# Performance work log

Hardware: AMD Instinct MI355X
Metric: run time of the kernel (lower is better)

Reference implementation:

```python
import jax, jax.numpy as jnp
import numpy as np

B, S, D = 4, 2048, 1024

def setup_inputs() -> dict:
    key = jax.random.key(0)
    ks = jax.random.split(key, 4)
    scale = 1.0 / np.sqrt(D)
    return {
        "x": jax.random.normal(ks[0], (B, S, D), dtype=jnp.float32),
        "Wq": jax.random.normal(ks[1], (D, D), dtype=jnp.float32) * scale,
        "bq": jnp.zeros((D,), dtype=jnp.float32),
        "Wk": jax.random.normal(ks[2], (D, D), dtype=jnp.float32) * scale,
        "bk": jnp.zeros((D,), dtype=jnp.float32),
        "Wv": jax.random.normal(ks[3], (D, D), dtype=jnp.float32) * scale,
        "bv": jnp.zeros((D,), dtype=jnp.float32),
    }

def reference(x, Wq, bq, Wk, bk, Wv, bv):
    d = x.shape[-1]
    Q = jnp.einsum('bsd,df->bsf', x, Wq) + bq  # [B,S,D]
    K = jnp.einsum('bsd,df->bsf', x, Wk) + bk
    V = jnp.einsum('bsd,df->bsf', x, Wv) + bv
    scores = jnp.einsum('bqd,bkd->bqk', Q, K) / jnp.sqrt(jnp.asarray(d, x.dtype))  # [B,S,S]
    weights = jax.nn.softmax(scores, axis=-1)
    return jnp.einsum('bqk,bkd->bqd', weights, V)  # [B,S,D]
```

## Files before the change

### kernel.cpp

```cpp
#include <hip/hip_runtime.h>
#include <stdint.h>


typedef __attribute__((ext_vector_type(8))) short bf16x8;
typedef __attribute__((ext_vector_type(4))) float f32x4;
typedef __attribute__((ext_vector_type(4))) unsigned short u16x4;
typedef __attribute__((ext_vector_type(8))) unsigned short u16x8;

__device__ __forceinline__ unsigned short f2bf(float f) {
  union { float f; unsigned u; } v; v.f = f;
  return (unsigned short)((v.u + 0x7FFFu + ((v.u >> 16) & 1u)) >> 16);
}
__device__ __forceinline__ unsigned short f2h(float f) {
  union { _Float16 h; unsigned short u; } v; v.h = (_Float16)f;
  return v.u;
}
__device__ __forceinline__ float h2f(unsigned short u) {
  union { unsigned short u; _Float16 h; } v; v.u = u;
  return (float)v.h;
}

__device__ __forceinline__ void gload16(const void* g, void* l) {
  __builtin_amdgcn_global_load_lds(
      (const __attribute__((address_space(1))) unsigned int*)g,
      (__attribute__((address_space(3))) unsigned int*)l, 16, 0, 0);
}

template <int N>
__device__ __forceinline__ void wait_vm() {
  asm volatile("s_waitcnt vmcnt(%0)" ::"n"(N) : "memory");
}

__device__ __forceinline__ int swz8(int bid, int cpx) {
  return (bid & 7) * cpx + (bid >> 3);
}

__device__ __forceinline__ f32x4 mfma16(bf16x8 a, bf16x8 b, f32x4 c) {
  return __builtin_amdgcn_mfma_f32_16x16x32_bf16(a, b, c, 0, 0, 0);
}

__device__ __forceinline__ void gemm_core(
    const unsigned short* __restrict__ A, const unsigned short* __restrict__ Bt,
    const int lda, const int ldb, const int nt,
    const long aRow0, const long bRow0, char* lds,
    f32x4 (&acc)[8][4]) {
  constexpr int A_BYTES = 256 * 64;
  constexpr int SLOT = A_BYTES + 128 * 64;
  constexpr int LA = 4, LB = 2, L = LA + LB;
  const int tid = threadIdx.x;
  const int lane = tid & 63;
  const int wid = tid >> 6;
  const int wm = wid >> 1, wn = wid & 1;
  const int l15 = lane & 15, lhi = lane >> 4;

  long goffA[LA]; int ldsoffA[LA];
#pragma unroll
  for (int j = 0; j < LA; ++j) {
    const int local = j * 4096 + tid * 16;
    const int row = local >> 6, ch = (local >> 4) & 3;
    goffA[j] = (aRow0 + row) * (long)lda + ((ch ^ ((row >> 1) & 3)) << 3);
    ldsoffA[j] = local;
  }
  long goffB[LB]; int ldsoffB[LB];
#pragma unroll
  for (int j = 0; j < LB; ++j) {
    const int local = j * 4096 + tid * 16;
    const int row = local >> 6, ch = (local >> 4) & 3;
    goffB[j] = (bRow0 + row) * (long)ldb + ((ch ^ ((row >> 1) & 3)) << 3);
    ldsoffB[j] = A_BYTES + local;
  }
  int raddrA[8];
#pragma unroll
  for (int m = 0; m < 8; ++m) {
    const int row = wm * 128 + m * 16 + l15;
    raddrA[m] = row * 64 + ((lhi ^ ((row >> 1) & 3)) << 4);
  }
  int raddrB[4];
#pragma unroll
  for (int n = 0; n < 4; ++n) {
    const int row = wn * 64 + n * 16 + l15;
    raddrB[n] = A_BYTES + row * 64 + ((lhi ^ ((row >> 1) & 3)) << 4);
  }

  const f32x4 z4 = {0.f, 0.f, 0.f, 0.f};
#pragma unroll
  for (int m = 0; m < 8; ++m)
#pragma unroll
    for (int n = 0; n < 4; ++n) acc[m][n] = z4;

  auto stage_tile = [&](int T) {
    char* dst = lds + (T % 3) * SLOT;
    const int k0 = T << 5;
#pragma unroll
    for (int j = 0; j < LA; ++j) gload16(A + goffA[j] + k0, dst + ldsoffA[j]);
#pragma unroll
    for (int j = 0; j < LB; ++j) gload16(Bt + goffB[j] + k0, dst + ldsoffB[j]);
  };

  stage_tile(0);
  stage_tile(1);
  wait_vm<L>();
  __builtin_amdgcn_s_barrier();

  for (int t = 0; t < nt; ++t) {
    const char* sb = lds + (t % 3) * SLOT;
    bf16x8 af[8], bfr[4];
#pragma unroll
    for (int n = 0; n < 4; ++n) bfr[n] = *(const bf16x8*)(sb + raddrB[n]);
#pragma unroll
    for (int m = 0; m < 8; ++m) af[m] = *(const bf16x8*)(sb + raddrA[m]);
    if (t + 2 < nt) stage_tile(t + 2);
    __builtin_amdgcn_s_setprio(1);
#pragma unroll
    for (int m = 0; m < 8; ++m)
#pragma unroll
      for (int n = 0; n < 4; ++n) acc[m][n] = mfma16(af[m], bfr[n], acc[m][n]);
    __builtin_amdgcn_s_setprio(0);
    if (t + 2 < nt) wait_vm<L>();
    else if (t + 1 < nt) wait_vm<0>();
    __builtin_amdgcn_s_barrier();
  }
}

__device__ __forceinline__ void gemm_core3(
    const unsigned short* __restrict__ A, const unsigned short* __restrict__ Bt,
    const int lda, const int ldb, const int nt64,
    const long aRow0, const long bRow0, char* lds,
    f32x4 (&acc)[8][4]) {
  constexpr int SLICE = 256 * 64;
  constexpr int A_BYTES = 2 * SLICE;
  constexpr int SLOT = 2 * A_BYTES;
  const int tid = threadIdx.x;
  const int lane = tid & 63;
  const int wid = tid >> 6;
  const int wm = wid >> 2, wn = wid & 3;
  const int l15 = lane & 15, lhi = lane >> 4;

  long goffA[2][2], goffB[2][2];
  int ldsoff[2];
#pragma unroll
  for (int j = 0; j < 2; ++j) {
    const int local = j * 8192 + tid * 16;
    const int row = local >> 6, ch = (local >> 4) & 3;
    ldsoff[j] = local;
    const int kalt = (ch ^ ((row >> 1) & 3)) << 3;
#pragma unroll
    for (int kk = 0; kk < 2; ++kk) {
      goffA[kk][j] = (aRow0 + row) * (long)lda + kk * 32 + kalt;
      goffB[kk][j] = (bRow0 + row) * (long)ldb + kk * 32 + kalt;
    }
  }
  int raddrA[8];
#pragma unroll
  for (int m = 0; m < 8; ++m) {
    const int row = wm * 128 + m * 16 + l15;
    raddrA[m] = row * 64 + ((lhi ^ ((row >> 1) & 3)) << 4);
  }
  int raddrB[4];
#pragma unroll
  for (int n = 0; n < 4; ++n) {
    const int row = wn * 64 + n * 16 + l15;
    raddrB[n] = row * 64 + ((lhi ^ ((row >> 1) & 3)) << 4);
  }

  const f32x4 z4 = {0.f, 0.f, 0.f, 0.f};
#pragma unroll
  for (int m = 0; m < 8; ++m)
#pragma unroll
    for (int n = 0; n < 4; ++n) acc[m][n] = z4;

  auto stageA = [&](int s, int kk, int T) {
    char* dst = lds + s * SLOT + kk * SLICE;
    const long k0 = (long)T << 6;
#pragma unroll
    for (int j = 0; j < 2; ++j) gload16(A + goffA[kk][j] + k0, dst + ldsoff[j]);
  };
  auto stageB = [&](int s, int kk, int T) {
    char* dst = lds + s * SLOT + A_BYTES + kk * SLICE;
    const long k0 = (long)T << 6;
#pragma unroll
    for (int j = 0; j < 2; ++j) gload16(Bt + goffB[kk][j] + k0, dst + ldsoff[j]);
  };

  stageA(0, 0, 0); stageB(0, 0, 0);
  stageA(0, 1, 0); stageB(0, 1, 0);
  wait_vm<4>();
  __builtin_amdgcn_s_barrier();

  int cur = 0;
  for (int t = 0; t < nt64; ++t) {
    const char* sb = lds + cur * SLOT;
    const int nxt = cur ^ 1;
    const bool pf = (t + 1 < nt64);
    bf16x8 a0[4], a1[4], b0[4], b1[4];
#pragma unroll
    for (int n = 0; n < 4; ++n) b0[n] = *(const bf16x8*)(sb + A_BYTES + raddrB[n]);
#pragma unroll
    for (int m = 0; m < 4; ++m) a0[m] = *(const bf16x8*)(sb + raddrA[m]);
    if (pf) stageA(nxt, 0, t + 1);
    __builtin_amdgcn_s_barrier();
    __builtin_amdgcn_s_setprio(1);
#pragma unroll
    for (int m = 0; m < 4; ++m)
#pragma unroll
      for (int n = 0; n < 4; ++n) acc[m][n] = mfma16(a0[m], b0[n], acc[m][n]);
    __builtin_amdgcn_s_setprio(0);
    __builtin_amdgcn_s_barrier();
#pragma unroll
    for (int m = 0; m < 4; ++m) a1[m] = *(const bf16x8*)(sb + raddrA[4 + m]);
    if (pf) { stageB(nxt, 0, t + 1); wait_vm<4>(); }
    else wait_vm<0>();
    __builtin_amdgcn_s_barrier();
    __builtin_amdgcn_s_setprio(1);
#pragma unroll
    for (int m = 0; m < 4; ++m)
#pragma unroll
      for (int n = 0; n < 4; ++n)
        acc[4 + m][n] = mfma16(a1[m], b0[n], acc[4 + m][n]);
    __builtin_amdgcn_s_setprio(0);
    __builtin_amdgcn_s_barrier();
#pragma unroll
    for (int n = 0; n < 4; ++n)
      b1[n] = *(const bf16x8*)(sb + A_BYTES + SLICE + raddrB[n]);
#pragma unroll
    for (int m = 0; m < 4; ++m) a0[m] = *(const bf16x8*)(sb + SLICE + raddrA[m]);
    if (pf) stageA(nxt, 1, t + 1);
    __builtin_amdgcn_s_barrier();
    __builtin_amdgcn_s_setprio(1);
#pragma unroll
    for (int m = 0; m < 4; ++m)
#pragma unroll
      for (int n = 0; n < 4; ++n) acc[m][n] = mfma16(a0[m], b1[n], acc[m][n]);
    __builtin_amdgcn_s_setprio(0);
    __builtin_amdgcn_s_barrier();
#pragma unroll
    for (int m = 0; m < 4; ++m)
      a1[m] = *(const bf16x8*)(sb + SLICE + raddrA[4 + m]);
    if (pf) { stageB(nxt, 1, t + 1); wait_vm<4>(); }
    __builtin_amdgcn_s_barrier();
    __builtin_amdgcn_s_setprio(1);
#pragma unroll
    for (int m = 0; m < 4; ++m)
#pragma unroll
      for (int n = 0; n < 4; ++n)
        acc[4 + m][n] = mfma16(a1[m], b1[n], acc[4 + m][n]);
    __builtin_amdgcn_s_setprio(0);
    __builtin_amdgcn_s_barrier();
    cur = nxt;
  }
}

__global__ __launch_bounds__(256, 2) void qkv_kernel(
    const unsigned short* __restrict__ X, const unsigned short* __restrict__ TQ,
    const unsigned short* __restrict__ TK, const unsigned short* __restrict__ TV,
    const float* __restrict__ bq, const float* __restrict__ bk,
    const float* __restrict__ bv, unsigned short* __restrict__ Q16,
    unsigned short* __restrict__ K16, unsigned short* __restrict__ VT) {
  __shared__ char lds[3 * 24576];
  const int wgid = swz8(blockIdx.x, 96);
  const int tm = wgid / 24, tn = wgid % 24;
  const int w = tn >> 3, c = tn & 7;
  const unsigned short* Bt = w == 0 ? TQ : (w == 1 ? TK : TV);
  const float* bias = w == 0 ? bq : (w == 1 ? bk : bv);

  f32x4 acc[8][4];
  gemm_core(X, Bt, 1024, 1024, 32, (long)tm * 256, (long)c * 128, lds, acc);

  const int tid = threadIdx.x, lane = tid & 63, wid = tid >> 6;
  const int wm = wid >> 1, wn = wid & 1;
  const int l15 = lane & 15, lhi = lane >> 4;
  const int rowBase = tm * 256 + wm * 128;
  const int colBase = c * 128 + wn * 64;
  if (w < 2) {
    unsigned short* C = w == 0 ? Q16 : K16;
#pragma unroll
    for (int m = 0; m < 8; ++m)
#pragma unroll
      for (int n = 0; n < 4; ++n) {
        const int col = colBase + n * 16 + l15;
        const float bvv = bias[col];
#pragma unroll
        for (int j = 0; j < 4; ++j) {
          const int row = rowBase + m * 16 + lhi * 4 + j;
          C[(long)row * 1024 + col] = f2bf(acc[m][n][j] + bvv);
        }
      }
  } else {
#pragma unroll
    for (int m = 0; m < 8; ++m)
#pragma unroll
      for (int n = 0; n < 4; ++n) {
        const int col = colBase + n * 16 + l15;
        const float bvv = bias[col];
        const int row0 = rowBase + m * 16 + lhi * 4;
        const int b = row0 >> 11, s = row0 & 2047;
        u16x4 v;
#pragma unroll
        for (int j = 0; j < 4; ++j) v[j] = f2bf(acc[m][n][j] + bvv);
        *reinterpret_cast<u16x4*>(&VT[(long)b * 2097152 + (long)col * 2048 + s]) = v;
      }
  }
}

__global__ __launch_bounds__(512, 1) void scores_kernel(
    const unsigned short* __restrict__ Q16, const unsigned short* __restrict__ K16,
    unsigned short* __restrict__ SC16) {
  extern __shared__ char lds[];
  const int wgid = swz8(blockIdx.x, 32);
  const int bz = wgid >> 6, tm = (wgid >> 3) & 7, tn = wgid & 7;
  const unsigned short* A = Q16 + (long)bz * 2097152;
  const unsigned short* Bt = K16 + (long)bz * 2097152;

  f32x4 acc[8][4];
  gemm_core3(A, Bt, 1024, 1024, 16, (long)tm * 256, (long)tn * 256, lds, acc);

  unsigned short* C = SC16 + (long)bz * 4194304;
  const int tid = threadIdx.x, lane = tid & 63, wid = tid >> 6;
  const int wm = wid >> 2, wn = wid & 3;
  const int l15 = lane & 15, lhi = lane >> 4;
  const int rowBase = tm * 256 + wm * 128;
  const int colBase = tn * 256 + wn * 64;
#pragma unroll
  for (int m = 0; m < 8; ++m)
#pragma unroll
    for (int n = 0; n < 4; ++n) {
      const int col = colBase + n * 16 + l15;
#pragma unroll
      for (int j = 0; j < 4; ++j) {
        const int row = rowBase + m * 16 + lhi * 4 + j;
        C[(long)row * 2048 + col] = f2h(acc[m][n][j] * (1.f / 32.f));
      }
    }
}

__global__ __launch_bounds__(256, 2) void pv_kernel(
    const unsigned short* __restrict__ P16, const unsigned short* __restrict__ VT,
    float* __restrict__ out) {
  __shared__ char lds[3 * 24576];
  const int wgid = swz8(blockIdx.x, 32);
  const int bz = wgid >> 6, tm = (wgid >> 3) & 7, tn = wgid & 7;
  const unsigned short* A = P16 + (long)bz * 4194304;
  const unsigned short* Bt = VT + (long)bz * 2097152;

  f32x4 acc[8][4];
  gemm_core(A, Bt, 2048, 2048, 64, (long)tm * 256, (long)tn * 128, lds, acc);

  float* C = out + (long)bz * 2097152;
  const int tid = threadIdx.x, lane = tid & 63, wid = tid >> 6;
  const int wm = wid >> 1, wn = wid & 1;
  const int l15 = lane & 15, lhi = lane >> 4;
  const int rowBase = tm * 256 + wm * 128;
  const int colBase = tn * 128 + wn * 64;
#pragma unroll
  for (int m = 0; m < 8; ++m)
#pragma unroll
    for (int n = 0; n < 4; ++n) {
      const int col = colBase + n * 16 + l15;
#pragma unroll
      for (int j = 0; j < 4; ++j) {
        const int row = rowBase + m * 16 + lhi * 4 + j;
        C[(long)row * 1024 + col] = acc[m][n][j];
      }
    }
}

__global__ __launch_bounds__(256) void cvt4(const float* __restrict__ in,
                                            unsigned short* __restrict__ out) {
  int i = blockIdx.x * 256 + threadIdx.x;
  float4 v = reinterpret_cast<const float4*>(in)[i];
  u16x4 r;
  r[0] = f2bf(v.x); r[1] = f2bf(v.y); r[2] = f2bf(v.z); r[3] = f2bf(v.w);
  reinterpret_cast<u16x4*>(out)[i] = r;
}

__global__ __launch_bounds__(256) void cvtWt(
    const float* __restrict__ w0, const float* __restrict__ w1, const float* __restrict__ w2,
    unsigned short* __restrict__ t0, unsigned short* __restrict__ t1, unsigned short* __restrict__ t2) {
  const float* w = blockIdx.y == 0 ? w0 : (blockIdx.y == 1 ? w1 : w2);
  unsigned short* t = blockIdx.y == 0 ? t0 : (blockIdx.y == 1 ? t1 : t2);
  int id = blockIdx.x * 256 + threadIdx.x;
  int k = id >> 10, n = id & 1023;
  t[n * 1024 + k] = f2bf(w[id]);
}

__global__ __launch_bounds__(256) void softmax_rows(const unsigned short* __restrict__ S,
                                                    unsigned short* __restrict__ P) {
  const long row = blockIdx.x;
  const u16x8* src = reinterpret_cast<const u16x8*>(S + row * 2048);
  const int tid = threadIdx.x;
  u16x8 a = src[tid];
  float v[8];
#pragma unroll
  for (int i = 0; i < 8; ++i) v[i] = h2f(a[i]);
  float m = v[0];
#pragma unroll
  for (int i = 1; i < 8; ++i) m = fmaxf(m, v[i]);
#pragma unroll
  for (int o = 32; o > 0; o >>= 1) m = fmaxf(m, __shfl_xor(m, o));
  __shared__ float red[8];
  const int wid = tid >> 6, lane = tid & 63;
  if (lane == 0) red[wid] = m;
  __syncthreads();
  m = fmaxf(fmaxf(red[0], red[1]), fmaxf(red[2], red[3]));
  float s = 0.f;
#pragma unroll
  for (int i = 0; i < 8; ++i) { v[i] = __expf(v[i] - m); s += v[i]; }
#pragma unroll
  for (int o = 32; o > 0; o >>= 1) s += __shfl_xor(s, o);
  if (lane == 0) red[4 + wid] = s;
  __syncthreads();
  s = (red[4] + red[5]) + (red[6] + red[7]);
  const float inv = 1.f / s;
  u16x8 p;
#pragma unroll
  for (int i = 0; i < 8; ++i) p[i] = f2bf(v[i] * inv);
  reinterpret_cast<u16x8*>(P + row * 2048)[tid] = p;
}

extern "C" void kernel_launch(void* const* d_in, const int* in_sizes, int n_in,
                              void* d_out, int out_size, void* d_ws, size_t ws_size,
                              hipStream_t stream) {
  const float* x  = (const float*)d_in[0];
  const float* Wq = (const float*)d_in[1];
  const float* bq = (const float*)d_in[2];
  const float* Wk = (const float*)d_in[3];
  const float* bk = (const float*)d_in[4];
  const float* Wv = (const float*)d_in[5];
  const float* bv = (const float*)d_in[6];
  float* out = (float*)d_out;

  char* ws = (char*)d_ws;
  const size_t MB = 1024 * 1024;
  unsigned short* X16 = (unsigned short*)(ws);
  unsigned short* TQ  = (unsigned short*)(ws + 16 * MB);
  unsigned short* TK  = (unsigned short*)(ws + 18 * MB);
  unsigned short* TV  = (unsigned short*)(ws + 20 * MB);
  unsigned short* Q16 = (unsigned short*)(ws + 22 * MB);
  unsigned short* K16 = (unsigned short*)(ws + 38 * MB);
  unsigned short* VT  = (unsigned short*)(ws + 54 * MB);
  unsigned short* SC16 = (unsigned short*)(ws + 70 * MB);
  unsigned short* P16 = Q16;

  static bool attr_set = false;
  if (!attr_set) {
    hipFuncSetAttribute(reinterpret_cast<const void*>(scores_kernel),
                        hipFuncAttributeMaxDynamicSharedMemorySize, 131072);
    attr_set = true;
  }

  cvt4<<<8192, 256, 0, stream>>>(x, X16);
  cvtWt<<<dim3(4096, 3), 256, 0, stream>>>(Wq, Wk, Wv, TQ, TK, TV);

  qkv_kernel<<<768, 256, 0, stream>>>(X16, TQ, TK, TV, bq, bk, bv, Q16, K16, VT);
  scores_kernel<<<256, 512, 131072, stream>>>(Q16, K16, SC16);
  softmax_rows<<<4 * 2048, 256, 0, stream>>>(SC16, P16);
  pv_kernel<<<256, 256, 0, stream>>>(P16, VT, out);

  (void)in_sizes; (void)n_in; (void)out_size; (void)ws_size;
}
```

Before: 174.4 us.

## Split PV tile across 8 waves and fuse conversion kernels into one launch

The PV GEMM moves from 256 threads holding 8x4 accumulator fragments per wave to 512 threads holding 4x4. The block tile stays 256x128, so each wave carries half the accumulators and the CU gets more waves to hide latency. A dedicated staging core splits the global-to-LDS loads for the new thread count. Separately, the x conversion and the weight-transpose conversion are merged into one kernel launch, with each weight block handling four elements per thread, to cut launch overhead. The cost is more LDS read traffic per MFMA in the PV loop, and the weight transpose still uses uncoalesced stores.

```diff
diff --git a/kernel.cpp b/kernel.cpp
--- a/kernel.cpp
+++ b/kernel.cpp
@@ -122,6 +122,87 @@
   }
 }
 
+__device__ __forceinline__ void gemm_core_pv(
+    const unsigned short* __restrict__ A, const unsigned short* __restrict__ Bt,
+    const int lda, const int ldb, const int nt,
+    const long aRow0, const long bRow0, char* lds,
+    f32x4 (&acc)[4][4]) {
+  constexpr int A_BYTES = 256 * 64;
+  constexpr int SLOT = A_BYTES + 128 * 64;
+  constexpr int LA = 2, LB = 1, L = LA + LB;
+  const int tid = threadIdx.x;
+  const int lane = tid & 63;
+  const int wid = tid >> 6;
+  const int wm = wid >> 1, wn = wid & 1;
+  const int l15 = lane & 15, lhi = lane >> 4;
+
+  long goffA[LA]; int ldsoffA[LA];
+#pragma unroll
+  for (int j = 0; j < LA; ++j) {
+    const int local = j * 8192 + tid * 16;
+    const int row = local >> 6, ch = (local >> 4) & 3;
+    goffA[j] = (aRow0 + row) * (long)lda + ((ch ^ ((row >> 1) & 3)) << 3);
+    ldsoffA[j] = local;
+  }
+  long goffB; int ldsoffB;
+  {
+    const int local = tid * 16;
+    const int row = local >> 6, ch = (local >> 4) & 3;
+    goffB = (bRow0 + row) * (long)ldb + ((ch ^ ((row >> 1) & 3)) << 3);
+    ldsoffB = A_BYTES + local;
+  }
+  int raddrA[4];
+#pragma unroll
+  for (int m = 0; m < 4; ++m) {
+    const int row = wm * 64 + m * 16 + l15;
+    raddrA[m] = row * 64 + ((lhi ^ ((row >> 1) & 3)) << 4);
+  }
+  int raddrB[4];
+#pragma unroll
+  for (int n = 0; n < 4; ++n) {
+    const int row = wn * 64 + n * 16 + l15;
+    raddrB[n] = A_BYTES + row * 64 + ((lhi ^ ((row >> 1) & 3)) << 4);
+  }
+
+  const f32x4 z4 = {0.f, 0.f, 0.f, 0.f};
+#pragma unroll
+  for (int m = 0; m < 4; ++m)
+#pragma unroll
+    for (int n = 0; n < 4; ++n) acc[m][n] = z4;
+
+  auto stage_tile = [&](int T) {
+    char* dst = lds + (T % 3) * SLOT;
+    const int k0 = T << 5;
+#pragma unroll
+    for (int j = 0; j < LA; ++j) gload16(A + goffA[j] + k0, dst + ldsoffA[j]);
+    gload16(Bt + goffB + k0, dst + ldsoffB);
+  };
+
+  stage_tile(0);
+  stage_tile(1);
+  wait_vm<L>();
+  __builtin_amdgcn_s_barrier();
+
+  for (int t = 0; t < nt; ++t) {
+    const char* sb = lds + (t % 3) * SLOT;
+    bf16x8 af[4], bfr[4];
+#pragma unroll
+    for (int n = 0; n < 4; ++n) bfr[n] = *(const bf16x8*)(sb + raddrB[n]);
+#pragma unroll
+    for (int m = 0; m < 4; ++m) af[m] = *(const bf16x8*)(sb + raddrA[m]);
+    if (t + 2 < nt) stage_tile(t + 2);
+    __builtin_amdgcn_s_setprio(1);
+#pragma unroll
+    for (int m = 0; m < 4; ++m)
+#pragma unroll
+      for (int n = 0; n < 4; ++n) acc[m][n] = mfma16(af[m], bfr[n], acc[m][n]);
+    __builtin_amdgcn_s_setprio(0);
+    if (t + 2 < nt) wait_vm<L>();
+    else if (t + 1 < nt) wait_vm<0>();
+    __builtin_amdgcn_s_barrier();
+  }
+}
+
 __device__ __forceinline__ void gemm_core3(
     const unsigned short* __restrict__ A, const unsigned short* __restrict__ Bt,
     const int lda, const int ldb, const int nt64,
@@ -333,7 +414,7 @@
     }
 }
 
-__global__ __launch_bounds__(256, 2) void pv_kernel(
+__global__ __launch_bounds__(512, 1) void pv_kernel(
     const unsigned short* __restrict__ P16, const unsigned short* __restrict__ VT,
     float* __restrict__ out) {
   __shared__ char lds[3 * 24576];
@@ -342,17 +423,17 @@
   const unsigned short* A = P16 + (long)bz * 4194304;
   const unsigned short* Bt = VT + (long)bz * 2097152;
 
-  f32x4 acc[8][4];
-  gemm_core(A, Bt, 2048, 2048, 64, (long)tm * 256, (long)tn * 128, lds, acc);
+  f32x4 acc[4][4];
+  gemm_core_pv(A, Bt, 2048, 2048, 64, (long)tm * 256, (long)tn * 128, lds, acc);
 
   float* C = out + (long)bz * 2097152;
   const int tid = threadIdx.x, lane = tid & 63, wid = tid >> 6;
   const int wm = wid >> 1, wn = wid & 1;
   const int l15 = lane & 15, lhi = lane >> 4;
-  const int rowBase = tm * 256 + wm * 128;
+  const int rowBase = tm * 256 + wm * 64;
   const int colBase = tn * 128 + wn * 64;
 #pragma unroll
-  for (int m = 0; m < 8; ++m)
+  for (int m = 0; m < 4; ++m)
 #pragma unroll
     for (int n = 0; n < 4; ++n) {
       const int col = colBase + n * 16 + l15;
@@ -364,23 +445,32 @@
     }
 }
 
-__global__ __launch_bounds__(256) void cvt4(const float* __restrict__ in,
-                                            unsigned short* __restrict__ out) {
-  int i = blockIdx.x * 256 + threadIdx.x;
-  float4 v = reinterpret_cast<const float4*>(in)[i];
-  u16x4 r;
-  r[0] = f2bf(v.x); r[1] = f2bf(v.y); r[2] = f2bf(v.z); r[3] = f2bf(v.w);
-  reinterpret_cast<u16x4*>(out)[i] = r;
-}
-
-__global__ __launch_bounds__(256) void cvtWt(
-    const float* __restrict__ w0, const float* __restrict__ w1, const float* __restrict__ w2,
-    unsigned short* __restrict__ t0, unsigned short* __restrict__ t1, unsigned short* __restrict__ t2) {
-  const float* w = blockIdx.y == 0 ? w0 : (blockIdx.y == 1 ? w1 : w2);
-  unsigned short* t = blockIdx.y == 0 ? t0 : (blockIdx.y == 1 ? t1 : t2);
-  int id = blockIdx.x * 256 + threadIdx.x;
-  int k = id >> 10, n = id & 1023;
-  t[n * 1024 + k] = f2bf(w[id]);
+__global__ __launch_bounds__(256) void cvt_all(
+    const float* __restrict__ x, unsigned short* __restrict__ X16,
+    const float* __restrict__ w0, const float* __restrict__ w1,
+    const float* __restrict__ w2, unsigned short* __restrict__ t0,
+    unsigned short* __restrict__ t1, unsigned short* __restrict__ t2) {
+  const int bid = blockIdx.x;
+  const int tid = threadIdx.x;
+  if (bid < 8192) {
+    int i = bid * 256 + tid;
+    float4 v = reinterpret_cast<const float4*>(x)[i];
+    u16x4 r;
+    r[0] = f2bf(v.x); r[1] = f2bf(v.y); r[2] = f2bf(v.z); r[3] = f2bf(v.w);
+    reinterpret_cast<u16x4*>(X16)[i] = r;
+  } else {
+    const int b2 = bid - 8192;
+    const int wsel = b2 >> 10, blk = b2 & 1023;
+    const float* w = wsel == 0 ? w0 : (wsel == 1 ? w1 : w2);
+    unsigned short* t = wsel == 0 ? t0 : (wsel == 1 ? t1 : t2);
+    const int base = blk * 1024;
+#pragma unroll
+    for (int e = 0; e < 4; ++e) {
+      const int id = base + e * 256 + tid;
+      const int k = id >> 10, n = id & 1023;
+      t[n * 1024 + k] = f2bf(w[id]);
+    }
+  }
 }
 
 __global__ __launch_bounds__(256) void softmax_rows(const unsigned short* __restrict__ S,
@@ -448,13 +538,12 @@
     attr_set = true;
   }
 
-  cvt4<<<8192, 256, 0, stream>>>(x, X16);
-  cvtWt<<<dim3(4096, 3), 256, 0, stream>>>(Wq, Wk, Wv, TQ, TK, TV);
+  cvt_all<<<11264, 256, 0, stream>>>(x, X16, Wq, Wk, Wv, TQ, TK, TV);
 
   qkv_kernel<<<768, 256, 0, stream>>>(X16, TQ, TK, TV, bq, bk, bv, Q16, K16, VT);
   scores_kernel<<<256, 512, 131072, stream>>>(Q16, K16, SC16);
   softmax_rows<<<4 * 2048, 256, 0, stream>>>(SC16, P16);
-  pv_kernel<<<256, 256, 0, stream>>>(P16, VT, out);
+  pv_kernel<<<256, 512, 0, stream>>>(P16, VT, out);
 
   (void)in_sizes; (void)n_in; (void)out_size; (void)ws_size;
 }
```

Measured after the change: 180.4 us. 1.03x slower.
